# Performance work log

Hardware: AMD Instinct MI355X
Metric: run time of the kernel (lower is better)

The kernel has to match this reference:

```python
import jax, jax.numpy as jnp
import numpy as np

B, T, F, H = 32, 2048, 768, 12
DH = F // H  # 64


def setup_inputs() -> dict:
    key = jax.random.key(0)
    ks = jax.random.split(key, 4)
    x = jax.random.normal(ks[0], (B, T, F), dtype=jnp.float32)
    mask = jnp.zeros((B, 1, T, 1), dtype=jnp.float32)
    W_attn = jax.random.normal(ks[1], (F, 3 * F), dtype=jnp.float32) * 0.02
    b_attn = jnp.zeros((1, 3 * F), dtype=jnp.float32)
    W_proj = jax.random.normal(ks[2], (F, F), dtype=jnp.float32) * 0.02
    b_proj = jnp.zeros((1, F), dtype=jnp.float32)
    return {"x": x, "mask": mask, "W_attn": W_attn, "b_attn": b_attn,
            "W_proj": W_proj, "b_proj": b_proj}


def _split_heads(t):
    # [B, T, F] -> [B, H, T, dh]
    b, s, f = t.shape
    return t.reshape(b, s, H, f // H).transpose(0, 2, 1, 3)


def _merge_heads(t):
    # [B, H, T, dh] -> [B, T, F]
    b, h, s, d = t.shape
    return t.transpose(0, 2, 1, 3).reshape(b, s, h * d)


def reference(x, mask, W_attn, b_attn, W_proj, b_proj):
    qkv = x @ W_attn + b_attn                      # [B, T, 3F]
    q, k, v = jnp.split(qkv, 3, axis=2)
    q, k, v = _split_heads(q), _split_heads(k), _split_heads(v)  # [B,H,T,dh]

    dk = jnp.asarray(DH, jnp.float32)
    # matmul(q, k, transpose_a=True): contract over T -> [B, H, dh, dh]
    w = jnp.einsum('bhtd,bhte->bhde', q, k) / jnp.sqrt(dk)
    # causal mask over feature axis (nd == ns == dh -> lower triangle)
    i = jnp.arange(DH)[:, None]
    j = jnp.arange(DH)[None, :]
    b = (i >= j).astype(w.dtype)                   # [dh, dh]
    w = w * b - 10000.0 * (1.0 - b)
    # matmul(w, v, transpose_b=True): [B,H,dh,dh] @ [B,H,dh,T] -> [B,H,dh,T]
    w = jnp.einsum('bhde,bhte->bhdt', w, v)
    w = w / (dk ** 4)
    w = w.transpose(0, 1, 3, 2)                    # [B, H, T, dh]
    w = w + mask                                   # mask broadcasts [B,1,T,1]
    w = jax.nn.softmax(w, axis=-2)                 # softmax over time axis
    # dropout is identity at inference (training=False)
    a = v * w                                      # elementwise, not matmul

    a = _merge_heads(a)                            # [B, T, F]
    w = _merge_heads(w)                            # [B, T, F]
    a = a @ W_proj + b_proj
    return (a, w)
```

## Files before the change

kernel.cpp:

```cpp
#include <hip/hip_runtime.h>

#define B_    32
#define T_    2048
#define F_    768
#define H_    12
#define DH_   64
#define MTOK  (B_*T_)
#define NQKV  (3*F_)

typedef __bf16 bf16;
typedef __bf16 bf16x8 __attribute__((ext_vector_type(8)));
typedef float  f32x4  __attribute__((ext_vector_type(4)));

__device__ __forceinline__ void gload_lds16(const bf16* g, bf16* l) {
  __builtin_amdgcn_global_load_lds(
      (const __attribute__((address_space(1))) unsigned*)g,
      (__attribute__((address_space(3))) unsigned*)l, 16, 0, 0);
}

__global__ void k_cast_x(const float* __restrict__ in, bf16* __restrict__ out, int n8) {
  int i = blockIdx.x * 256 + threadIdx.x;
  if (i >= n8) return;
  const float4* p = (const float4*)in + (size_t)i * 2;
  float4 f0 = p[0], f1 = p[1];
  bf16x8 o;
  o[0]=(bf16)f0.x; o[1]=(bf16)f0.y; o[2]=(bf16)f0.z; o[3]=(bf16)f0.w;
  o[4]=(bf16)f1.x; o[5]=(bf16)f1.y; o[6]=(bf16)f1.z; o[7]=(bf16)f1.w;
  *((bf16x8*)out + i) = o;
}

__global__ void k_tcast(const float* __restrict__ in, bf16* __restrict__ out, int K, int N) {
  __shared__ float tile[32][33];
  int n0 = blockIdx.x * 32, k0 = blockIdx.y * 32;
  int tx = threadIdx.x & 31, ty = threadIdx.x >> 5;
#pragma unroll
  for (int r = 0; r < 4; ++r)
    tile[ty + r*8][tx] = in[(size_t)(k0 + ty + r*8) * N + n0 + tx];
  __syncthreads();
#pragma unroll
  for (int r = 0; r < 4; ++r)
    out[(size_t)(n0 + ty + r*8) * K + k0 + tx] = (bf16)tile[tx][ty + r*8];
}

template <typename OutT>
__global__ void k_gemm_bt(const bf16* __restrict__ A, const bf16* __restrict__ Bt,
                          const float* __restrict__ bias, OutT* __restrict__ C,
                          int M, int N, int K, int Mt) {
  __shared__ bf16 As[128 * 32];
  __shared__ bf16 Bs[128 * 32];
  int nwg = gridDim.x;
  int bid = blockIdx.x;
  int swz = (bid & 7) * (nwg >> 3) + (bid >> 3);
  int bm = swz % Mt, bn = swz / Mt;
  int tid = threadIdx.x, wv = tid >> 6, l = tid & 63;
  int wm = (wv >> 1) * 64, wn = (wv & 1) * 64;
  f32x4 acc[4][4] = {};
  const bf16* Ab = A + (size_t)(bm * 128) * K;
  const bf16* Bb = Bt + (size_t)(bn * 128) * K;
  int srow = l >> 2;
  int scol = (l & 3) * 8;
  const int nk = K >> 5;
  for (int kt = 0; kt < nk; ++kt) {
    int k0 = kt * 32;
    __syncthreads();
#pragma unroll
    for (int i = 0; i < 2; ++i) {
      int rr = (i * 4 + wv) * 16 + srow;
      gload_lds16(Ab + (size_t)rr * K + k0 + scol, As + (i * 4 + wv) * 512);
      gload_lds16(Bb + (size_t)rr * K + k0 + scol, Bs + (i * 4 + wv) * 512);
    }
    __syncthreads();
    bf16x8 af[4], bfr[4];
#pragma unroll
    for (int t = 0; t < 4; ++t) {
      af[t]  = *(const bf16x8*)&As[(wm + t * 16 + (l & 15)) * 32 + (l >> 4) * 8];
      bfr[t] = *(const bf16x8*)&Bs[(wn + t * 16 + (l & 15)) * 32 + (l >> 4) * 8];
    }
#pragma unroll
    for (int mi = 0; mi < 4; ++mi)
#pragma unroll
      for (int ni = 0; ni < 4; ++ni)
        acc[mi][ni] = __builtin_amdgcn_mfma_f32_16x16x32_bf16(af[mi], bfr[ni], acc[mi][ni], 0, 0, 0);
  }
#pragma unroll
  for (int ni = 0; ni < 4; ++ni) {
    int col = bn * 128 + wn + ni * 16 + (l & 15);
    float bv = bias[col];
#pragma unroll
    for (int mi = 0; mi < 4; ++mi)
#pragma unroll
      for (int r = 0; r < 4; ++r) {
        int row = bm * 128 + wm + mi * 16 + (l >> 4) * 4 + r;
        C[(size_t)row * N + col] = (OutT)(acc[mi][ni][r] + bv);
      }
  }
}

__global__ void k_stage2_partial(const bf16* __restrict__ qkv, float* __restrict__ Spart) {
  int bid = blockIdx.x;
  int part = bid & 3, bh = bid >> 2;
  int b = bh / H_, h = bh % H_;
  __shared__ float qs[64][68];
  __shared__ float ks[64][68];
  int tid = threadIdx.x;
  int d0 = (tid >> 4) * 4, e0 = (tid & 15) * 4;
  int sr = tid >> 2, sc = (tid & 3) * 16;
  const bf16* qb = qkv + (size_t)b * T_ * NQKV + h * DH_;
  const bf16* kb = qb + F_;
  float acc[4][4] = {};
  for (int tc = part * 512; tc < part * 512 + 512; tc += 64) {
    __syncthreads();
    bf16x8 qv0 = *(const bf16x8*)&qb[(size_t)(tc + sr) * NQKV + sc];
    bf16x8 qv1 = *(const bf16x8*)&qb[(size_t)(tc + sr) * NQKV + sc + 8];
    bf16x8 kv0 = *(const bf16x8*)&kb[(size_t)(tc + sr) * NQKV + sc];
    bf16x8 kv1 = *(const bf16x8*)&kb[(size_t)(tc + sr) * NQKV + sc + 8];
#pragma unroll
    for (int j = 0; j < 8; ++j) {
      qs[sr][sc + j] = (float)qv0[j]; qs[sr][sc + 8 + j] = (float)qv1[j];
      ks[sr][sc + j] = (float)kv0[j]; ks[sr][sc + 8 + j] = (float)kv1[j];
    }
    __syncthreads();
#pragma unroll 4
    for (int t = 0; t < 64; ++t) {
      f32x4 q4 = *(const f32x4*)&qs[t][d0];
      f32x4 k4 = *(const f32x4*)&ks[t][e0];
#pragma unroll
      for (int i = 0; i < 4; ++i)
#pragma unroll
        for (int j = 0; j < 4; ++j)
          acc[i][j] = fmaf(q4[i], k4[j], acc[i][j]);
    }
  }
  float* Sp = Spart + (size_t)(part * 384 + bh) * 4096;
#pragma unroll
  for (int i = 0; i < 4; ++i)
#pragma unroll
    for (int j = 0; j < 4; ++j)
      Sp[(d0 + i) * 64 + e0 + j] = acc[i][j];
}

__global__ void k_stage2_finish(const float* __restrict__ Spart, bf16* __restrict__ S2b) {
  int bh = blockIdx.x;
  const float sc_keep = 0.125f / 16777216.0f;
  const float sc_mask = -10000.0f / 16777216.0f;
  for (int i = threadIdx.x; i < 4096; i += 256) {
    int d = i >> 6, e = i & 63;
    float s = 0.f;
#pragma unroll
    for (int p = 0; p < 4; ++p) s += Spart[(size_t)(p * 384 + bh) * 4096 + i];
    float v = (e <= d) ? s * sc_keep : sc_mask;
    S2b[(size_t)bh * 4096 + i] = (bf16)v;
  }
}

__global__ __launch_bounds__(256) void k_stage3(const bf16* __restrict__ qkv,
                                                const bf16* __restrict__ S2b,
                                                const float* __restrict__ mask,
                                                float* __restrict__ w_out,
                                                bf16* __restrict__ a_pre) {
  int bh = blockIdx.x;
  int b = bh / H_, h = bh % H_;
  int tid = threadIdx.x, wv = tid >> 6, l = tid & 63;
  const bf16* S2 = S2b + (size_t)bh * 4096;
  bf16x8 sfrag[2][4];
#pragma unroll
  for (int ks = 0; ks < 2; ++ks)
#pragma unroll
    for (int n = 0; n < 4; ++n)
      sfrag[ks][n] = *(const bf16x8*)&S2[(n * 16 + (l & 15)) * 64 + ks * 32 + (l >> 4) * 8];
  const bf16* vb = qkv + (size_t)b * T_ * NQKV + 2 * F_ + h * DH_;
  const float* mb = mask + (size_t)b * T_;
  int t_lo = wv * 512;

  float se[4] = {0.f, 0.f, 0.f, 0.f};
  for (int t0 = t_lo; t0 < t_lo + 512; t0 += 16) {
    f32x4 acc[4] = {};
    bf16x8 a0 = *(const bf16x8*)&vb[(size_t)(t0 + (l & 15)) * NQKV + (l >> 4) * 8];
    bf16x8 a1 = *(const bf16x8*)&vb[(size_t)(t0 + (l & 15)) * NQKV + 32 + (l >> 4) * 8];
#pragma unroll
    for (int n = 0; n < 4; ++n) {
      acc[n] = __builtin_amdgcn_mfma_f32_16x16x32_bf16(a0, sfrag[0][n], acc[n], 0, 0, 0);
      acc[n] = __builtin_amdgcn_mfma_f32_16x16x32_bf16(a1, sfrag[1][n], acc[n], 0, 0, 0);
    }
    float4 mv = *(const float4*)&mb[t0 + (l >> 4) * 4];
    float mr[4] = {mv.x, mv.y, mv.z, mv.w};
#pragma unroll
    for (int n = 0; n < 4; ++n)
#pragma unroll
      for (int r = 0; r < 4; ++r)
        se[n] += __expf(acc[n][r] + mr[r]);
  }
#pragma unroll
  for (int n = 0; n < 4; ++n) {
    se[n] += __shfl_xor(se[n], 16, 64);
    se[n] += __shfl_xor(se[n], 32, 64);
  }
  __shared__ float sred[4][64];
  __shared__ float inv[64];
  if (l < 16) {
#pragma unroll
    for (int n = 0; n < 4; ++n) sred[wv][n * 16 + l] = se[n];
  }
  __syncthreads();
  if (tid < 64) inv[tid] = 1.0f / (sred[0][tid] + sred[1][tid] + sred[2][tid] + sred[3][tid]);
  __syncthreads();
  float iv[4];
#pragma unroll
  for (int n = 0; n < 4; ++n) iv[n] = inv[n * 16 + (l & 15)];

  for (int t0 = t_lo; t0 < t_lo + 512; t0 += 16) {
    f32x4 acc[4] = {};
    bf16x8 a0 = *(const bf16x8*)&vb[(size_t)(t0 + (l & 15)) * NQKV + (l >> 4) * 8];
    bf16x8 a1 = *(const bf16x8*)&vb[(size_t)(t0 + (l & 15)) * NQKV + 32 + (l >> 4) * 8];
#pragma unroll
    for (int n = 0; n < 4; ++n) {
      acc[n] = __builtin_amdgcn_mfma_f32_16x16x32_bf16(a0, sfrag[0][n], acc[n], 0, 0, 0);
      acc[n] = __builtin_amdgcn_mfma_f32_16x16x32_bf16(a1, sfrag[1][n], acc[n], 0, 0, 0);
    }
    float4 mv = *(const float4*)&mb[t0 + (l >> 4) * 4];
    float mr[4] = {mv.x, mv.y, mv.z, mv.w};
#pragma unroll
    for (int r = 0; r < 4; ++r) {
      int t = t0 + (l >> 4) * 4 + r;
      size_t orow = ((size_t)b * T_ + t) * F_ + h * DH_;
#pragma unroll
      for (int n = 0; n < 4; ++n) {
        int dd = n * 16 + (l & 15);
        float w = __expf(acc[n][r] + mr[r]) * iv[n];
        w_out[orow + dd] = w;
        float vval = (float)vb[(size_t)t * NQKV + dd];
        a_pre[orow + dd] = (bf16)(vval * w);
      }
    }
  }
}

extern "C" void kernel_launch(void* const* d_in, const int* in_sizes, int n_in,
                              void* d_out, int out_size, void* d_ws, size_t ws_size,
                              hipStream_t stream) {
  const float* x      = (const float*)d_in[0];
  const float* mask   = (const float*)d_in[1];
  const float* W_attn = (const float*)d_in[2];
  const float* b_attn = (const float*)d_in[3];
  const float* W_proj = (const float*)d_in[4];
  const float* b_proj = (const float*)d_in[5];
  float* out_a = (float*)d_out;
  float* out_w = out_a + (size_t)MTOK * F_;

  char* ws = (char*)d_ws;
  bf16*  qkv   = (bf16*)(ws + 0);
  bf16*  xb    = (bf16*)(ws + 301989888ull);
  bf16*  waT   = (bf16*)(ws + 402653184ull);
  bf16*  wpT   = (bf16*)(ws + 406192128ull);
  float* Spart = (float*)(ws + 407371776ull);
  bf16*  S2b   = (bf16*)(ws + 432537600ull);
  bf16*  a_pre = xb;

  k_cast_x<<<24576, 256, 0, stream>>>(x, xb, MTOK * F_ / 8);
  k_tcast<<<dim3(NQKV / 32, F_ / 32), 256, 0, stream>>>(W_attn, waT, F_, NQKV);
  k_tcast<<<dim3(F_ / 32, F_ / 32), 256, 0, stream>>>(W_proj, wpT, F_, F_);
  k_gemm_bt<bf16><<<(MTOK / 128) * (NQKV / 128), 256, 0, stream>>>(
      xb, waT, b_attn, qkv, MTOK, NQKV, F_, MTOK / 128);
  k_stage2_partial<<<B_ * H_ * 4, 256, 0, stream>>>(qkv, Spart);
  k_stage2_finish<<<B_ * H_, 256, 0, stream>>>(Spart, S2b);
  k_stage3<<<B_ * H_, 256, 0, stream>>>(qkv, S2b, mask, out_w, a_pre);
  k_gemm_bt<float><<<(MTOK / 128) * (F_ / 128), 256, 0, stream>>>(
      a_pre, wpT, b_proj, out_a, MTOK, F_, F_, MTOK / 128);
}
```

Baseline: 1.244 ms.

## Use MFMA for Q^T K reduction in one kernel and reorder GEMM tile mapping

Replaces the two-kernel FP32 Q^T·K reduction (partial sums over four time chunks, then a finish kernel) with a single kernel per (batch, head). Each wave runs bf16 MFMA over its own quarter of time, and the four wave results are summed in LDS before the causal mask and scaling are applied. This removes the fp32 partial-sum buffer round trip and one launch, but the per-element strided bf16 global loads may be poorly coalesced, and the grid shrinks to 384 blocks. The GEMM tile index mapping also switches from M-major to N-major, so adjacent workgroups share A rows for better cache reuse.

```diff
diff --git a/kernel.cpp b/kernel.cpp
--- a/kernel.cpp
+++ b/kernel.cpp
@@ -45,13 +45,13 @@
 template <typename OutT>
 __global__ void k_gemm_bt(const bf16* __restrict__ A, const bf16* __restrict__ Bt,
                           const float* __restrict__ bias, OutT* __restrict__ C,
-                          int M, int N, int K, int Mt) {
+                          int M, int N, int K, int Nt) {
   __shared__ bf16 As[128 * 32];
   __shared__ bf16 Bs[128 * 32];
   int nwg = gridDim.x;
   int bid = blockIdx.x;
   int swz = (bid & 7) * (nwg >> 3) + (bid >> 3);
-  int bm = swz % Mt, bn = swz / Mt;
+  int bn = swz % Nt, bm = swz / Nt;
   int tid = threadIdx.x, wv = tid >> 6, l = tid & 63;
   int wm = (wv >> 1) * 64, wn = (wv & 1) * 64;
   f32x4 acc[4][4] = {};
@@ -96,60 +96,59 @@
   }
 }
 
-__global__ void k_stage2_partial(const bf16* __restrict__ qkv, float* __restrict__ Spart) {
-  int bid = blockIdx.x;
-  int part = bid & 3, bh = bid >> 2;
+__global__ __launch_bounds__(256) void k_stage2(const bf16* __restrict__ qkv,
+                                                bf16* __restrict__ S2b) {
+  int bh = blockIdx.x;
   int b = bh / H_, h = bh % H_;
-  __shared__ float qs[64][68];
-  __shared__ float ks[64][68];
-  int tid = threadIdx.x;
-  int d0 = (tid >> 4) * 4, e0 = (tid & 15) * 4;
-  int sr = tid >> 2, sc = (tid & 3) * 16;
+  int tid = threadIdx.x, wv = tid >> 6, l = tid & 63;
   const bf16* qb = qkv + (size_t)b * T_ * NQKV + h * DH_;
   const bf16* kb = qb + F_;
-  float acc[4][4] = {};
-  for (int tc = part * 512; tc < part * 512 + 512; tc += 64) {
+  f32x4 acc[4][4] = {};
+  int tbase = wv * 512 + (l >> 4) * 8;
+  int dcol = l & 15;
+  for (int kt = 0; kt < 16; ++kt) {
+    int t0 = tbase + kt * 32;
+    bf16x8 af[4], bfv[4];
+#pragma unroll
+    for (int j = 0; j < 8; ++j) {
+      const bf16* qrow = qb + (size_t)(t0 + j) * NQKV;
+      const bf16* krow = kb + (size_t)(t0 + j) * NQKV;
+#pragma unroll
+      for (int di = 0; di < 4; ++di) {
+        af[di][j]  = qrow[di * 16 + dcol];
+        bfv[di][j] = krow[di * 16 + dcol];
+      }
+    }
+#pragma unroll
+    for (int di = 0; di < 4; ++di)
+#pragma unroll
+      for (int ej = 0; ej < 4; ++ej)
+        acc[di][ej] = __builtin_amdgcn_mfma_f32_16x16x32_bf16(af[di], bfv[ej], acc[di][ej], 0, 0, 0);
+  }
+  __shared__ float Sred[64][68];
+  for (int w = 0; w < 4; ++w) {
+    if (wv == w) {
+#pragma unroll
+      for (int di = 0; di < 4; ++di)
+#pragma unroll
+        for (int ej = 0; ej < 4; ++ej)
+#pragma unroll
+          for (int r = 0; r < 4; ++r) {
+            int d = di * 16 + (l >> 4) * 4 + r;
+            int e = ej * 16 + dcol;
+            if (w == 0) Sred[d][e] = acc[di][ej][r];
+            else        Sred[d][e] += acc[di][ej][r];
+          }
+    }
     __syncthreads();
-    bf16x8 qv0 = *(const bf16x8*)&qb[(size_t)(tc + sr) * NQKV + sc];
-    bf16x8 qv1 = *(const bf16x8*)&qb[(size_t)(tc + sr) * NQKV + sc + 8];
-    bf16x8 kv0 = *(const bf16x8*)&kb[(size_t)(tc + sr) * NQKV + sc];
-    bf16x8 kv1 = *(const bf16x8*)&kb[(size_t)(tc + sr) * NQKV + sc + 8];
-#pragma unroll
-    for (int j = 0; j < 8; ++j) {
-      qs[sr][sc + j] = (float)qv0[j]; qs[sr][sc + 8 + j] = (float)qv1[j];
-      ks[sr][sc + j] = (float)kv0[j]; ks[sr][sc + 8 + j] = (float)kv1[j];
-    }
-    __syncthreads();
-#pragma unroll 4
-    for (int t = 0; t < 64; ++t) {
-      f32x4 q4 = *(const f32x4*)&qs[t][d0];
-      f32x4 k4 = *(const f32x4*)&ks[t][e0];
-#pragma unroll
-      for (int i = 0; i < 4; ++i)
-#pragma unroll
-        for (int j = 0; j < 4; ++j)
-          acc[i][j] = fmaf(q4[i], k4[j], acc[i][j]);
-    }
-  }
-  float* Sp = Spart + (size_t)(part * 384 + bh) * 4096;
-#pragma unroll
-  for (int i = 0; i < 4; ++i)
-#pragma unroll
-    for (int j = 0; j < 4; ++j)
-      Sp[(d0 + i) * 64 + e0 + j] = acc[i][j];
-}
-
-__global__ void k_stage2_finish(const float* __restrict__ Spart, bf16* __restrict__ S2b) {
-  int bh = blockIdx.x;
+  }
   const float sc_keep = 0.125f / 16777216.0f;
   const float sc_mask = -10000.0f / 16777216.0f;
-  for (int i = threadIdx.x; i < 4096; i += 256) {
+  bf16* out = S2b + (size_t)bh * 4096;
+  for (int i = tid; i < 4096; i += 256) {
     int d = i >> 6, e = i & 63;
-    float s = 0.f;
-#pragma unroll
-    for (int p = 0; p < 4; ++p) s += Spart[(size_t)(p * 384 + bh) * 4096 + i];
-    float v = (e <= d) ? s * sc_keep : sc_mask;
-    S2b[(size_t)bh * 4096 + i] = (bf16)v;
+    float v = (e <= d) ? Sred[d][e] * sc_keep : sc_mask;
+    out[i] = (bf16)v;
   }
 }
 
@@ -252,7 +251,6 @@
   bf16*  xb    = (bf16*)(ws + 301989888ull);
   bf16*  waT   = (bf16*)(ws + 402653184ull);
   bf16*  wpT   = (bf16*)(ws + 406192128ull);
-  float* Spart = (float*)(ws + 407371776ull);
   bf16*  S2b   = (bf16*)(ws + 432537600ull);
   bf16*  a_pre = xb;
 
@@ -260,10 +258,9 @@
   k_tcast<<<dim3(NQKV / 32, F_ / 32), 256, 0, stream>>>(W_attn, waT, F_, NQKV);
   k_tcast<<<dim3(F_ / 32, F_ / 32), 256, 0, stream>>>(W_proj, wpT, F_, F_);
   k_gemm_bt<bf16><<<(MTOK / 128) * (NQKV / 128), 256, 0, stream>>>(
-      xb, waT, b_attn, qkv, MTOK, NQKV, F_, MTOK / 128);
-  k_stage2_partial<<<B_ * H_ * 4, 256, 0, stream>>>(qkv, Spart);
-  k_stage2_finish<<<B_ * H_, 256, 0, stream>>>(Spart, S2b);
+      xb, waT, b_attn, qkv, MTOK, NQKV, F_, NQKV / 128);
+  k_stage2<<<B_ * H_, 256, 0, stream>>>(qkv, S2b);
   k_stage3<<<B_ * H_, 256, 0, stream>>>(qkv, S2b, mask, out_w, a_pre);
   k_gemm_bt<float><<<(MTOK / 128) * (F_ / 128), 256, 0, stream>>>(
-      a_pre, wpT, b_proj, out_a, MTOK, F_, F_, MTOK / 128);
-}
+      a_pre, wpT, b_proj, out_a, MTOK, F_, F_, F_ / 128);
+}
```

Result: faster. 1.169 ms (-6.1%).
